# Kernel tuning notes

Measured on AMD Instinct MI355X. Metric: run time of the kernel, lower is better.

## Reference

```python
import jax, jax.numpy as jnp
import numpy as np

N = 3072        # seeds = 3 * batch (src, dst, neg)
K = 64          # num_tokens (sampled neighbors per seed)
C = 128         # edge_dim (mixer channels)
T = 100         # time_dim
ND = 128        # node_dim
ED = 128        # embed_dim
NUM_NODES = 100000
TG = 98304      # total flattened time-gap neighbor indices
L = 2           # num mixer layers
TH = int(K * 0.5)   # token hidden = 32
CH = int(C * 4.0)   # channel hidden = 512
PAD = 0         # PADDED_NODE_ID


def setup_inputs() -> dict:
    key = jax.random.key(0)
    ks = jax.random.split(key, 32)
    inp = {}
    inp['edge_feat'] = jax.random.normal(ks[0], (N, K, C), jnp.float32)
    inp['seed_times'] = jax.random.uniform(ks[1], (N,), jnp.float32) * 1000.0
    inp['nbr_time'] = jax.random.uniform(ks[2], (N, K), jnp.float32) * 1000.0
    inp['node_feat'] = jax.random.normal(ks[3], (NUM_NODES, ND), jnp.float32)
    # Time2Vec frozen frequencies (GraphMixer style)
    inp['time_w'] = jnp.asarray(1.0 / np.power(10.0, np.linspace(0.0, 9.0, T)), jnp.float32)
    s = 0.02
    inp['proj_W'] = jax.random.normal(ks[4], (C + T, C), jnp.float32) * s
    inp['proj_b'] = jnp.zeros((C,), jnp.float32)
    inp['ln1_g'] = jnp.ones((L, C), jnp.float32)
    inp['ln1_b'] = jnp.zeros((L, C), jnp.float32)
    inp['tW1'] = jax.random.normal(ks[5], (L, K, TH), jnp.float32) * s
    inp['tb1'] = jnp.zeros((L, TH), jnp.float32)
    inp['tW2'] = jax.random.normal(ks[6], (L, TH, K), jnp.float32) * s
    inp['tb2'] = jnp.zeros((L, K), jnp.float32)
    inp['ln2_g'] = jnp.ones((L, C), jnp.float32)
    inp['ln2_b'] = jnp.zeros((L, C), jnp.float32)
    inp['cW1'] = jax.random.normal(ks[7], (L, C, CH), jnp.float32) * s
    inp['cb1'] = jnp.zeros((L, CH), jnp.float32)
    inp['cW2'] = jax.random.normal(ks[8], (L, CH, C), jnp.float32) * s
    inp['cb2'] = jnp.zeros((L, C), jnp.float32)
    inp['out_W'] = jax.random.normal(ks[9], (C + ND, ED), jnp.float32) * s
    inp['out_b'] = jnp.zeros((ED,), jnp.float32)
    inp['nbr_nids'] = jax.random.randint(ks[10], (N, K), 0, NUM_NODES, jnp.int32)
    inp['tg_idx'] = jax.random.randint(ks[11], (TG,), 0, NUM_NODES, jnp.int32)
    inp['tg_seg'] = jnp.sort(jax.random.randint(ks[12], (TG,), 0, N, jnp.int32))
    inp['seed_ids'] = jax.random.randint(ks[13], (N,), 0, NUM_NODES, jnp.int32)
    return inp


def _ln(x, g, b):
    m = jnp.mean(x, axis=-1, keepdims=True)
    v = jnp.var(x, axis=-1, keepdims=True)
    return (x - m) * jax.lax.rsqrt(v + 1e-5) * g + b


def reference(edge_feat, seed_times, nbr_time, node_feat, time_w, proj_W, proj_b,
              ln1_g, ln1_b, tW1, tb1, tW2, tb2, ln2_g, ln2_b, cW1, cb1, cW2, cb2,
              out_W, out_b, nbr_nids, tg_idx, tg_seg, seed_ids):
    # Time2Vec on time deltas: [N, K, T]
    dt = seed_times[:, None] - nbr_time
    tfeat = jnp.cos(dt[..., None] * time_w)
    # projection: [N, K, C]
    z = jnp.concatenate([edge_feat, tfeat], axis=-1) @ proj_W + proj_b
    # MLP-Mixer layers (token mixing over K, channel mixing over C)
    for l in range(L):
        h = _ln(z, ln1_g[l], ln1_b[l])
        h = jnp.einsum('nkc,kh->nhc', h, tW1[l]) + tb1[l][None, :, None]
        h = jax.nn.gelu(h)
        h = jnp.einsum('nhc,hk->nkc', h, tW2[l]) + tb2[l][None, :, None]
        z = z + h
        h = _ln(z, ln2_g[l], ln2_b[l])
        h = jax.nn.gelu(h @ cW1[l] + cb1[l]) @ cW2[l] + cb2[l]
        z = z + h
    # masked mean over valid neighbors -> [N, C]
    mask = (nbr_nids != PAD).astype(z.dtype)
    z = jnp.sum(z * mask[..., None], axis=1) / jnp.clip(jnp.sum(mask, axis=1, keepdims=True), 1.0)
    # ragged segment-mean over time-gap neighbors (replaces Python loop)
    counts = jax.ops.segment_sum(jnp.ones((TG,), z.dtype), tg_seg, num_segments=N)
    tg_feat = jax.ops.segment_sum(node_feat[tg_idx], tg_seg, num_segments=N) / jnp.clip(counts, 1.0)[:, None]
    z_node = tg_feat + node_feat[seed_ids]
    return jnp.concatenate([z, z_node], axis=1) @ out_W + out_b
```

## Files before the change

### kernel.cpp

```cpp
#include <hip/hip_runtime.h>
#include <math.h>

#define NS   3072
#define KT   64
#define CC   128
#define TDIM 100
#define TGN  98304
#define TH   32
#define CH   512
#define PS   136
#define PSA  136
#define PSK  72
#define PSH  40

typedef __attribute__((ext_vector_type(8))) short bf16x8;
typedef __attribute__((ext_vector_type(4))) float f32x4;

__device__ __forceinline__ unsigned short f2bf(float f) {
    unsigned int u = __float_as_uint(f);
    return (unsigned short)((u + 0x7FFFu + ((u >> 16) & 1u)) >> 16);
}
__device__ __forceinline__ float fast_exp2(float x) {
    float r; asm("v_exp_f32 %0, %1" : "=v"(r) : "v"(x)); return r;
}
__device__ __forceinline__ float fast_rcp(float x) {
    float r; asm("v_rcp_f32 %0, %1" : "=v"(r) : "v"(x)); return r;
}
__device__ __forceinline__ float fast_cos2pi(float rev) {
    float f = rev - floorf(rev);
    float r; asm("v_cos_f32 %0, %1" : "=v"(r) : "v"(f)); return r;
}
__device__ __forceinline__ unsigned int pk_bf16(float lo, float hi) {
    unsigned int r; asm("v_cvt_pk_bf16_f32 %0, %1, %2" : "=v"(r) : "v"(lo), "v"(hi)); return r;
}
__device__ __forceinline__ float gelu_f(float x) {
    float p = x * x;
    float e = fast_exp2(-x * fmaf(p, 0.1029436f, 2.3022082f));
    return x * fast_rcp(1.0f + e);
}

__global__ __launch_bounds__(256)
void gm_trans(const float* __restrict__ cW1, const float* __restrict__ cW2,
              const float* __restrict__ proj_W,
              unsigned short* __restrict__ cW1Tb, unsigned short* __restrict__ cW2Tb,
              unsigned short* __restrict__ projWTb)
{
    __shared__ float tile[32][33];
    const int bid = blockIdx.x;
    const float* src; unsigned short* dst;
    int R, Cs, oC, tr, tc;
    if (bid < 128) {
        int l = bid >> 6, q = bid & 63; tr = q >> 4; tc = q & 15;
        src = cW1 + l * CC * CH; dst = cW1Tb + l * CH * CC; R = CC; Cs = CH; oC = CC;
    } else if (bid < 256) {
        int b = bid - 128, l = b >> 6, q = b & 63; tr = q & 15; tc = q >> 4;
        src = cW2 + l * CH * CC; dst = cW2Tb + l * CC * CH; R = CH; Cs = CC; oC = CH;
    } else {
        int b = bid - 256; tr = b >> 2; tc = b & 3;
        src = proj_W; dst = projWTb; R = 228; Cs = CC; oC = 256;
    }
    const int tx = threadIdx.x & 31, ty0 = threadIdx.x >> 5;
    #pragma unroll
    for (int i = 0; i < 4; ++i) {
        int ty = ty0 + i * 8;
        int rr = tr * 32 + ty, cc = tc * 32 + tx;
        tile[ty][tx] = (rr < R) ? src[rr * Cs + cc] : 0.0f;
    }
    __syncthreads();
    #pragma unroll
    for (int i = 0; i < 4; ++i) {
        int ty = ty0 + i * 8;
        int orow = tc * 32 + ty, ocol = tr * 32 + tx;
        dst[orow * oC + ocol] = f2bf(tile[tx][ty]);
    }
}

__global__ __launch_bounds__(256)
void gm_prep_small(const float* __restrict__ tW1, const float* __restrict__ tW2,
                   unsigned short* __restrict__ tW1Tb, unsigned short* __restrict__ tW2Tb)
{
    int e = blockIdx.x * 256 + threadIdx.x;
    if (e < 4096) {
        int l = e >> 11, rem = e & 2047, h = rem >> 6, k = rem & 63;
        tW1Tb[e] = f2bf(tW1[(l * KT + k) * TH + h]);
    } else {
        int e2 = e - 4096, l = e2 >> 11, rem = e2 & 2047, k = rem >> 5, h = rem & 31;
        tW2Tb[e2] = f2bf(tW2[(l * TH + h) * KT + k]);
    }
}

__global__ __launch_bounds__(256, 3)
void gm_mixer(const float* __restrict__ edge_feat,
              const float* __restrict__ seed_times,
              const float* __restrict__ nbr_time,
              const float* __restrict__ time_w,
              const float* __restrict__ proj_b,
              const float* __restrict__ ln1_g, const float* __restrict__ ln1_b,
              const float* __restrict__ tb1,   const float* __restrict__ tb2,
              const float* __restrict__ ln2_g, const float* __restrict__ ln2_b,
              const float* __restrict__ cb1,   const float* __restrict__ cb2,
              const int*   __restrict__ nbr_nids,
              const unsigned short* __restrict__ projWTb,
              const unsigned short* __restrict__ tW1Tb,
              const unsigned short* __restrict__ tW2Tb,
              const unsigned short* __restrict__ cW1Tb,
              const unsigned short* __restrict__ cW2Tb,
              float* __restrict__ zmean)
{
    __shared__ short ubuf[17408];
    __shared__ float lnS[256], lnS2[256];
    __shared__ float mArr[KT], rArr[KT], maskArr[KT], dtArr[KT];

    const int n  = blockIdx.x;
    const int t  = threadIdx.x;
    const int w  = t >> 6;
    const int l  = t & 63;
    const int lr = l & 15;
    const int kg = l >> 4;
    const int c0 = w * 32 + lr;
    const int c1 = c0 + 16;

    short* Ab    = ubuf;
    short* LNz1T = ubuf;
    short* G2T   = ubuf + 128 * PSK;
    short* LNzb  = ubuf;
    short* Gb    = ubuf + 64 * PS;

    const f32x4 zero4 = {0.f, 0.f, 0.f, 0.f};
    f32x4 zr[4][2];

    if (t < KT) {
        dtArr[t]   = seed_times[n] - nbr_time[n * KT + t];
        maskArr[t] = (nbr_nids[n * KT + t] != 0) ? 1.0f : 0.0f;
    }
    {
        const float4* ef4 = (const float4*)(edge_feat + (size_t)n * KT * CC);
        #pragma unroll
        for (int it = 0; it < 8; ++it) {
            int i4 = it * 256 + t;
            int k = i4 >> 5, c = (i4 & 31) << 2;
            float4 v = ef4[i4];
            uint2 pk; pk.x = pk_bf16(v.x, v.y); pk.y = pk_bf16(v.z, v.w);
            *(uint2*)&Ab[k * PSA + c] = pk;
        }
    }
    __syncthreads();

    {
        f32x4 acc[4][2];
        #pragma unroll
        for (int mt = 0; mt < 4; ++mt) { acc[mt][0] = zero4; acc[mt][1] = zero4; }
        #pragma unroll
        for (int p = 0; p < 2; ++p) {
            #pragma unroll
            for (int ks = 0; ks < 4; ++ks) {
                const unsigned short* bp = projWTb + (w * 32 + lr) * 256 + p * 128 + ks * 32 + kg * 8;
                bf16x8 b0 = *(const bf16x8*)bp;
                bf16x8 b1 = *(const bf16x8*)(bp + 16 * 256);
                #pragma unroll
                for (int mt = 0; mt < 4; ++mt) {
                    bf16x8 a = *(const bf16x8*)&Ab[(mt * 16 + lr) * PSA + ks * 32 + kg * 8];
                    acc[mt][0] = __builtin_amdgcn_mfma_f32_16x16x32_bf16(a, b0, acc[mt][0], 0, 0, 0);
                    acc[mt][1] = __builtin_amdgcn_mfma_f32_16x16x32_bf16(a, b1, acc[mt][1], 0, 0, 0);
                }
            }
            if (p == 0) {
                __syncthreads();
                #pragma unroll
                for (int it = 0; it < 16; ++it) {
                    int idx = it * 256 + t;
                    int k = idx >> 6, j2 = (idx & 63) << 1;
                    unsigned pk = 0;
                    if (j2 < TDIM) {
                        float dt = dtArr[k];
                        float2 twv = *(const float2*)&time_w[j2];
                        pk = pk_bf16(fast_cos2pi(dt * twv.x * 0.15915494309f),
                                     fast_cos2pi(dt * twv.y * 0.15915494309f));
                    }
                    *(unsigned*)&Ab[k * PSA + j2] = pk;
                }
                __syncthreads();
            }
        }
        #pragma unroll
        for (int mt = 0; mt < 4; ++mt)
            #pragma unroll
            for (int nt = 0; nt < 2; ++nt) {
                float pb = proj_b[nt ? c1 : c0];
                #pragma unroll
                for (int r = 0; r < 4; ++r) zr[mt][nt][r] = acc[mt][nt][r] + pb;
            }
    }

    for (int lay = 0; lay < 2; ++lay) {
        #pragma unroll
        for (int mt = 0; mt < 4; ++mt) {
            f32x4 sv, qv;
            #pragma unroll
            for (int r = 0; r < 4; ++r) {
                float z0 = zr[mt][0][r], z1 = zr[mt][1][r];
                sv[r] = z0 + z1;
                qv[r] = z0 * z0 + z1 * z1;
            }
            #pragma unroll
            for (int d = 1; d < 16; d <<= 1)
                #pragma unroll
                for (int r = 0; r < 4; ++r) {
                    sv[r] += __shfl_xor(sv[r], d);
                    qv[r] += __shfl_xor(qv[r], d);
                }
            if (lr == 0) {
                *(f32x4*)&lnS [w * 64 + mt * 16 + kg * 4] = sv;
                *(f32x4*)&lnS2[w * 64 + mt * 16 + kg * 4] = qv;
            }
        }
        __syncthreads();
        if (t < KT) {
            float s  = lnS [t] + lnS [64 + t] + lnS [128 + t] + lnS [192 + t];
            float s2 = lnS2[t] + lnS2[64 + t] + lnS2[128 + t] + lnS2[192 + t];
            float m = s * (1.0f / CC);
            float var = s2 * (1.0f / CC) - m * m;
            mArr[t] = m; rArr[t] = rsqrtf(var + 1e-5f);
        }
        __syncthreads();

        {
            const float* g1 = ln1_g + lay * CC;
            const float* b1 = ln1_b + lay * CC;
            float gc0 = g1[c0], bc0 = b1[c0], gc1 = g1[c1], bc1 = b1[c1];
            #pragma unroll
            for (int mt = 0; mt < 4; ++mt) {
                f32x4 mv = *(const f32x4*)&mArr[mt * 16 + kg * 4];
                f32x4 rv = *(const f32x4*)&rArr[mt * 16 + kg * 4];
                #pragma unroll
                for (int nt = 0; nt < 2; ++nt) {
                    float gg = nt ? gc1 : gc0, bb = nt ? bc1 : bc0;
                    int c = nt ? c1 : c0;
                    float v0 = (zr[mt][nt][0] - mv[0]) * rv[0] * gg + bb;
                    float v1 = (zr[mt][nt][1] - mv[1]) * rv[1] * gg + bb;
                    float v2 = (zr[mt][nt][2] - mv[2]) * rv[2] * gg + bb;
                    float v3 = (zr[mt][nt][3] - mv[3]) * rv[3] * gg + bb;
                    uint2 pk; pk.x = pk_bf16(v0, v1); pk.y = pk_bf16(v2, v3);
                    *(uint2*)&LNz1T[c * PSK + mt * 16 + kg * 4] = pk;
                }
            }
        }

        {
            f32x4 acc1[2][2];
            #pragma unroll
            for (int mt = 0; mt < 2; ++mt) { acc1[mt][0] = zero4; acc1[mt][1] = zero4; }
            #pragma unroll
            for (int ks = 0; ks < 2; ++ks) {
                bf16x8 bb0 = *(const bf16x8*)&LNz1T[c0 * PSK + ks * 32 + kg * 8];
                bf16x8 bb1 = *(const bf16x8*)&LNz1T[c1 * PSK + ks * 32 + kg * 8];
                #pragma unroll
                for (int mt = 0; mt < 2; ++mt) {
                    bf16x8 a = *(const bf16x8*)&tW1Tb[lay * 2048 + (mt * 16 + lr) * 64 + ks * 32 + kg * 8];
                    acc1[mt][0] = __builtin_amdgcn_mfma_f32_16x16x32_bf16(a, bb0, acc1[mt][0], 0, 0, 0);
                    acc1[mt][1] = __builtin_amdgcn_mfma_f32_16x16x32_bf16(a, bb1, acc1[mt][1], 0, 0, 0);
                }
            }
            #pragma unroll
            for (int mt = 0; mt < 2; ++mt) {
                float4 tbv = *(const float4*)&tb1[lay * TH + mt * 16 + kg * 4];
                #pragma unroll
                for (int nt = 0; nt < 2; ++nt) {
                    int c = nt ? c1 : c0;
                    float g0 = gelu_f(acc1[mt][nt][0] + tbv.x);
                    float g1v = gelu_f(acc1[mt][nt][1] + tbv.y);
                    float g2 = gelu_f(acc1[mt][nt][2] + tbv.z);
                    float g3 = gelu_f(acc1[mt][nt][3] + tbv.w);
                    uint2 pk; pk.x = pk_bf16(g0, g1v); pk.y = pk_bf16(g2, g3);
                    *(uint2*)&G2T[c * PSH + mt * 16 + kg * 4] = pk;
                }
            }
        }
        {
            bf16x8 bb0 = *(const bf16x8*)&G2T[c0 * PSH + kg * 8];
            bf16x8 bb1 = *(const bf16x8*)&G2T[c1 * PSH + kg * 8];
            #pragma unroll
            for (int mt = 0; mt < 4; ++mt) {
                f32x4 a2v0 = zero4, a2v1 = zero4;
                bf16x8 a = *(const bf16x8*)&tW2Tb[lay * 2048 + (mt * 16 + lr) * 32 + kg * 8];
                a2v0 = __builtin_amdgcn_mfma_f32_16x16x32_bf16(a, bb0, a2v0, 0, 0, 0);
                a2v1 = __builtin_amdgcn_mfma_f32_16x16x32_bf16(a, bb1, a2v1, 0, 0, 0);
                float4 t2v = *(const float4*)&tb2[lay * KT + mt * 16 + kg * 4];
                #pragma unroll
                for (int r = 0; r < 4; ++r) {
                    float tb = (r == 0) ? t2v.x : (r == 1) ? t2v.y : (r == 2) ? t2v.z : t2v.w;
                    zr[mt][0][r] += a2v0[r] + tb;
                    zr[mt][1][r] += a2v1[r] + tb;
                }
            }
        }

        #pragma unroll
        for (int mt = 0; mt < 4; ++mt) {
            f32x4 sv, qv;
            #pragma unroll
            for (int r = 0; r < 4; ++r) {
                float z0 = zr[mt][0][r], z1 = zr[mt][1][r];
                sv[r] = z0 + z1;
                qv[r] = z0 * z0 + z1 * z1;
            }
            #pragma unroll
            for (int d = 1; d < 16; d <<= 1)
                #pragma unroll
                for (int r = 0; r < 4; ++r) {
                    sv[r] += __shfl_xor(sv[r], d);
                    qv[r] += __shfl_xor(qv[r], d);
                }
            if (lr == 0) {
                *(f32x4*)&lnS [w * 64 + mt * 16 + kg * 4] = sv;
                *(f32x4*)&lnS2[w * 64 + mt * 16 + kg * 4] = qv;
            }
        }
        __syncthreads();
        if (t < KT) {
            float s  = lnS [t] + lnS [64 + t] + lnS [128 + t] + lnS [192 + t];
            float s2 = lnS2[t] + lnS2[64 + t] + lnS2[128 + t] + lnS2[192 + t];
            float m = s * (1.0f / CC);
            float var = s2 * (1.0f / CC) - m * m;
            mArr[t] = m; rArr[t] = rsqrtf(var + 1e-5f);
        }
        __syncthreads();

        {
            const float* g2 = ln2_g + lay * CC;
            const float* b2 = ln2_b + lay * CC;
            float gc0 = g2[c0], bc0 = b2[c0], gc1 = g2[c1], bc1 = b2[c1];
            const bool odd = lr & 1;
            const int cb = odd ? (c1 - 1) : c0;
            #pragma unroll
            for (int mt = 0; mt < 4; ++mt) {
                f32x4 mv = *(const f32x4*)&mArr[mt * 16 + kg * 4];
                f32x4 rv = *(const f32x4*)&rArr[mt * 16 + kg * 4];
                #pragma unroll
                for (int r = 0; r < 4; ++r) {
                    float v0 = (zr[mt][0][r] - mv[r]) * rv[r] * gc0 + bc0;
                    float v1 = (zr[mt][1][r] - mv[r]) * rv[r] * gc1 + bc1;
                    float s0 = __shfl_xor(v0, 1);
                    float s1 = __shfl_xor(v1, 1);
                    unsigned pka = pk_bf16(v0, s0);
                    unsigned pkb = pk_bf16(s1, v1);
                    unsigned pkv = odd ? pkb : pka;
                    *(unsigned*)&LNzb[(mt * 16 + kg * 4 + r) * PS + cb] = pkv;
                }
            }
        }
        __syncthreads();

        {
            f32x4 accB[4][2];
            #pragma unroll
            for (int mt = 0; mt < 4; ++mt) { accB[mt][0] = zero4; accB[mt][1] = zero4; }

            for (int jc = 0; jc < 4; ++jc) {
                f32x4 accA[4][2];
                #pragma unroll
                for (int mt = 0; mt < 4; ++mt) { accA[mt][0] = zero4; accA[mt][1] = zero4; }
                #pragma unroll
                for (int ks = 0; ks < 4; ++ks) {
                    const unsigned short* w1p = cW1Tb + lay * CH * CC
                                              + (jc * 128 + w * 32 + lr) * CC + ks * 32 + kg * 8;
                    bf16x8 a0 = *(const bf16x8*)w1p;
                    bf16x8 a1 = *(const bf16x8*)(w1p + 16 * CC);
                    #pragma unroll
                    for (int mt = 0; mt < 4; ++mt) {
                        bf16x8 b = *(const bf16x8*)&LNzb[(mt * 16 + lr) * PS + ks * 32 + kg * 8];
                        accA[mt][0] = __builtin_amdgcn_mfma_f32_16x16x32_bf16(a0, b, accA[mt][0], 0, 0, 0);
                        accA[mt][1] = __builtin_amdgcn_mfma_f32_16x16x32_bf16(a1, b, accA[mt][1], 0, 0, 0);
                    }
                }
                #pragma unroll
                for (int nt = 0; nt < 2; ++nt) {
                    int j0 = w * 32 + nt * 16 + kg * 4;
                    float4 cbv = *(const float4*)&cb1[lay * CH + jc * 128 + j0];
                    #pragma unroll
                    for (int mt = 0; mt < 4; ++mt) {
                        float g0 = gelu_f(accA[mt][nt][0] + cbv.x);
                        float g1v = gelu_f(accA[mt][nt][1] + cbv.y);
                        float g2 = gelu_f(accA[mt][nt][2] + cbv.z);
                        float g3 = gelu_f(accA[mt][nt][3] + cbv.w);
                        uint2 pk; pk.x = pk_bf16(g0, g1v); pk.y = pk_bf16(g2, g3);
                        *(uint2*)&Gb[(mt * 16 + lr) * PS + j0] = pk;
                    }
                }
                __syncthreads();
                #pragma unroll
                for (int ks = 0; ks < 4; ++ks) {
                    const unsigned short* w2p = cW2Tb + lay * CC * CH
                                              + (w * 32 + lr) * CH + jc * 128 + ks * 32 + kg * 8;
                    bf16x8 b0 = *(const bf16x8*)w2p;
                    bf16x8 b1 = *(const bf16x8*)(w2p + 16 * CH);
                    #pragma unroll
                    for (int mt = 0; mt < 4; ++mt) {
                        bf16x8 a = *(const bf16x8*)&Gb[(mt * 16 + lr) * PS + ks * 32 + kg * 8];
                        accB[mt][0] = __builtin_amdgcn_mfma_f32_16x16x32_bf16(a, b0, accB[mt][0], 0, 0, 0);
                        accB[mt][1] = __builtin_amdgcn_mfma_f32_16x16x32_bf16(a, b1, accB[mt][1], 0, 0, 0);
                    }
                }
                __syncthreads();
            }
            #pragma unroll
            for (int mt = 0; mt < 4; ++mt)
                #pragma unroll
                for (int nt = 0; nt < 2; ++nt) {
                    float cb = cb2[lay * CC + (nt ? c1 : c0)];
                    #pragma unroll
                    for (int r = 0; r < 4; ++r) zr[mt][nt][r] += accB[mt][nt][r] + cb;
                }
        }
    }

    {
        float msum = 0.f, a0v = 0.f, a1v = 0.f;
        #pragma unroll
        for (int mt = 0; mt < 4; ++mt) {
            f32x4 mk4 = *(const f32x4*)&maskArr[mt * 16 + kg * 4];
            #pragma unroll
            for (int r = 0; r < 4; ++r) {
                msum += mk4[r];
                a0v  += zr[mt][0][r] * mk4[r];
                a1v  += zr[mt][1][r] * mk4[r];
            }
        }
        a0v  += __shfl_xor(a0v, 16);  a0v  += __shfl_xor(a0v, 32);
        a1v  += __shfl_xor(a1v, 16);  a1v  += __shfl_xor(a1v, 32);
        msum += __shfl_xor(msum, 16); msum += __shfl_xor(msum, 32);
        if (kg == 0) {
            float inv = fast_rcp(fmaxf(msum, 1.0f));
            zmean[n * CC + c0] = a0v * inv;
            zmean[n * CC + c1] = a1v * inv;
        }
    }
}

__global__ __launch_bounds__(256)
void gm_out(const float* __restrict__ zmean,
            const float* __restrict__ node_feat,
            const float* __restrict__ out_W,
            const float* __restrict__ out_b,
            const int*   __restrict__ tg_idx,
            const int*   __restrict__ tg_seg,
            const int*   __restrict__ seed_ids,
            float* __restrict__ outp)
{
    __shared__ float redf[8 * 132];
    __shared__ float zmL[CC], znL[CC], oL[2 * CC];
    const int n = blockIdx.x;
    const int t = threadIdx.x;
    const int q = t & 31, g = t >> 5;

    int a = 0, b = TGN;
    while (a < b) { int mm = (a + b) >> 1; if (tg_seg[mm] < n) a = mm + 1; else b = mm; }
    const int lo = a;
    int a2 = lo, b2 = TGN;
    while (a2 < b2) { int mm = (a2 + b2) >> 1; if (tg_seg[mm] < n + 1) a2 = mm + 1; else b2 = mm; }
    const int hi = a2;

    float4 acc = {0.f, 0.f, 0.f, 0.f};
    for (int i = lo + g; i < hi; i += 8) {
        int nid = tg_idx[i];
        const float4* nf = (const float4*)(node_feat + (size_t)nid * CC);
        float4 v = nf[q];
        acc.x += v.x; acc.y += v.y; acc.z += v.z; acc.w += v.w;
    }
    *(float4*)&redf[g * 132 + q * 4] = acc;
    __syncthreads();
    if (t < CC) {
        float s = 0.f;
        #pragma unroll
        for (int gg = 0; gg < 8; ++gg) s += redf[gg * 132 + t];
        float cnt = (float)(hi - lo);
        znL[t] = s / fmaxf(cnt, 1.0f) + node_feat[(size_t)seed_ids[n] * CC + t];
        zmL[t] = zmean[n * CC + t];
    }
    __syncthreads();
    {
        const int c = t & 127, h = t >> 7;
        const float* src = h ? znL : zmL;
        const float* Wp  = out_W + (size_t)h * CC * 128;
        float o = 0.f;
        for (int j = 0; j < CC; ++j) o += src[j] * Wp[j * 128 + c];
        oL[h * 128 + c] = o;
    }
    __syncthreads();
    if (t < CC) outp[n * 128 + t] = oL[t] + oL[CC + t] + out_b[t];
}

extern "C" void kernel_launch(void* const* d_in, const int* in_sizes, int n_in,
                              void* d_out, int out_size, void* d_ws, size_t ws_size,
                              hipStream_t stream)
{
    const float* edge_feat  = (const float*)d_in[0];
    const float* seed_times = (const float*)d_in[1];
    const float* nbr_time   = (const float*)d_in[2];
    const float* node_feat  = (const float*)d_in[3];
    const float* time_w     = (const float*)d_in[4];
    const float* proj_W     = (const float*)d_in[5];
    const float* proj_b     = (const float*)d_in[6];
    const float* ln1_g      = (const float*)d_in[7];
    const float* ln1_b      = (const float*)d_in[8];
    const float* tW1        = (const float*)d_in[9];
    const float* tb1        = (const float*)d_in[10];
    const float* tW2        = (const float*)d_in[11];
    const float* tb2        = (const float*)d_in[12];
    const float* ln2_g      = (const float*)d_in[13];
    const float* ln2_b      = (const float*)d_in[14];
    const float* cW1        = (const float*)d_in[15];
    const float* cb1        = (const float*)d_in[16];
    const float* cW2        = (const float*)d_in[17];
    const float* cb2        = (const float*)d_in[18];
    const float* out_W      = (const float*)d_in[19];
    const float* out_b      = (const float*)d_in[20];
    const int*   nbr_nids   = (const int*)d_in[21];
    const int*   tg_idx     = (const int*)d_in[22];
    const int*   tg_seg     = (const int*)d_in[23];
    const int*   seed_ids   = (const int*)d_in[24];

    char* ws = (char*)d_ws;
    float*          zmean   = (float*)ws;
    unsigned short* projWTb = (unsigned short*)(ws + 1572864);
    unsigned short* tW1Tb   = (unsigned short*)(ws + 1638400);
    unsigned short* tW2Tb   = (unsigned short*)(ws + 1646592);
    unsigned short* cW1Tb   = (unsigned short*)(ws + 1654784);
    unsigned short* cW2Tb   = (unsigned short*)(ws + 1916928);

    gm_trans<<<288, 256, 0, stream>>>(cW1, cW2, proj_W, cW1Tb, cW2Tb, projWTb);
    gm_prep_small<<<32, 256, 0, stream>>>(tW1, tW2, tW1Tb, tW2Tb);
    gm_mixer<<<NS, 256, 0, stream>>>(edge_feat, seed_times, nbr_time, time_w,
                                     proj_b, ln1_g, ln1_b, tb1, tb2, ln2_g, ln2_b,
                                     cb1, cb2, nbr_nids,
                                     projWTb, tW1Tb, tW2Tb, cW1Tb, cW2Tb, zmean);
    gm_out<<<NS, 256, 0, stream>>>(zmean, node_feat, out_W, out_b,
                                   tg_idx, tg_seg, seed_ids, (float*)d_out);
}
```

Measured before the change: 524.0 us.

## Fuse output stage into mixer, merge prep kernels, precompute segment offsets

Merges the two weight-prep kernels into one launch that also precomputes per-seed segment start offsets via binary search. The output gather, segment-mean and final projection are folded into the tail of the mixer kernel, which reuses its shared buffer, so the zmean round-trip through global memory and one launch go away. The mixer's occupancy hint is raised from 3 to 4 blocks per SM, and MFMA loops are wrapped in s_setprio to favour matrix issue. The fused tail adds a serial gather/GEMV phase to each mixer block, and the tighter launch bound may cause register spills.

```diff
diff --git a/kernel.cpp b/kernel.cpp
--- a/kernel.cpp
+++ b/kernel.cpp
@@ -40,13 +40,33 @@
 }
 
 __global__ __launch_bounds__(256)
-void gm_trans(const float* __restrict__ cW1, const float* __restrict__ cW2,
-              const float* __restrict__ proj_W,
-              unsigned short* __restrict__ cW1Tb, unsigned short* __restrict__ cW2Tb,
-              unsigned short* __restrict__ projWTb)
+void gm_prep(const float* __restrict__ cW1, const float* __restrict__ cW2,
+             const float* __restrict__ proj_W,
+             const float* __restrict__ tW1, const float* __restrict__ tW2,
+             const int*   __restrict__ tg_seg,
+             unsigned short* __restrict__ cW1Tb, unsigned short* __restrict__ cW2Tb,
+             unsigned short* __restrict__ projWTb,
+             unsigned short* __restrict__ tW1Tb, unsigned short* __restrict__ tW2Tb,
+             int* __restrict__ seg_lo)
 {
     __shared__ float tile[32][33];
     const int bid = blockIdx.x;
+    if (bid >= 288) {
+        int e = (bid - 288) * 256 + threadIdx.x;
+        if (e < 4096) {
+            int l = e >> 11, rem = e & 2047, h = rem >> 6, k = rem & 63;
+            tW1Tb[e] = f2bf(tW1[(l * KT + k) * TH + h]);
+        } else if (e < 8192) {
+            int e2 = e - 4096, l = e2 >> 11, rem = e2 & 2047, k = rem >> 5, h = rem & 31;
+            tW2Tb[e2] = f2bf(tW2[(l * TH + h) * KT + k]);
+        } else if (e < 8192 + 3073) {
+            int nn = e - 8192;
+            int a = 0, b = TGN;
+            while (a < b) { int mm = (a + b) >> 1; if (tg_seg[mm] < nn) a = mm + 1; else b = mm; }
+            seg_lo[nn] = a;
+        }
+        return;
+    }
     const float* src; unsigned short* dst;
     int R, Cs, oC, tr, tc;
     if (bid < 128) {
@@ -75,21 +95,7 @@
     }
 }
 
-__global__ __launch_bounds__(256)
-void gm_prep_small(const float* __restrict__ tW1, const float* __restrict__ tW2,
-                   unsigned short* __restrict__ tW1Tb, unsigned short* __restrict__ tW2Tb)
-{
-    int e = blockIdx.x * 256 + threadIdx.x;
-    if (e < 4096) {
-        int l = e >> 11, rem = e & 2047, h = rem >> 6, k = rem & 63;
-        tW1Tb[e] = f2bf(tW1[(l * KT + k) * TH + h]);
-    } else {
-        int e2 = e - 4096, l = e2 >> 11, rem = e2 & 2047, k = rem >> 5, h = rem & 31;
-        tW2Tb[e2] = f2bf(tW2[(l * TH + h) * KT + k]);
-    }
-}
-
-__global__ __launch_bounds__(256, 3)
+__global__ __launch_bounds__(256, 4)
 void gm_mixer(const float* __restrict__ edge_feat,
               const float* __restrict__ seed_times,
               const float* __restrict__ nbr_time,
@@ -105,7 +111,13 @@
               const unsigned short* __restrict__ tW2Tb,
               const unsigned short* __restrict__ cW1Tb,
               const unsigned short* __restrict__ cW2Tb,
-              float* __restrict__ zmean)
+              const float* __restrict__ node_feat,
+              const float* __restrict__ out_W,
+              const float* __restrict__ out_b,
+              const int*   __restrict__ tg_idx,
+              const int*   __restrict__ seed_ids,
+              const int*   __restrict__ seg_lo,
+              float* __restrict__ outp)
 {
     __shared__ short ubuf[17408];
     __shared__ float lnS[256], lnS2[256];
@@ -360,6 +372,7 @@
                 f32x4 accA[4][2];
                 #pragma unroll
                 for (int mt = 0; mt < 4; ++mt) { accA[mt][0] = zero4; accA[mt][1] = zero4; }
+                __builtin_amdgcn_s_setprio(1);
                 #pragma unroll
                 for (int ks = 0; ks < 4; ++ks) {
                     const unsigned short* w1p = cW1Tb + lay * CH * CC
@@ -373,6 +386,7 @@
                         accA[mt][1] = __builtin_amdgcn_mfma_f32_16x16x32_bf16(a1, b, accA[mt][1], 0, 0, 0);
                     }
                 }
+                __builtin_amdgcn_s_setprio(0);
                 #pragma unroll
                 for (int nt = 0; nt < 2; ++nt) {
                     int j0 = w * 32 + nt * 16 + kg * 4;
@@ -388,6 +402,7 @@
                     }
                 }
                 __syncthreads();
+                __builtin_amdgcn_s_setprio(1);
                 #pragma unroll
                 for (int ks = 0; ks < 4; ++ks) {
                     const unsigned short* w2p = cW2Tb + lay * CC * CH
@@ -401,6 +416,7 @@
                         accB[mt][1] = __builtin_amdgcn_mfma_f32_16x16x32_bf16(a, b1, accB[mt][1], 0, 0, 0);
                     }
                 }
+                __builtin_amdgcn_s_setprio(0);
                 __syncthreads();
             }
             #pragma unroll
@@ -413,6 +429,11 @@
                 }
         }
     }
+
+    float* redf = (float*)ubuf;
+    float* zmL  = redf + 8 * 132;
+    float* znL  = zmL + 128;
+    float* oL   = znL + 128;
 
     {
         float msum = 0.f, a0v = 0.f, a1v = 0.f;
@@ -431,43 +452,22 @@
         msum += __shfl_xor(msum, 16); msum += __shfl_xor(msum, 32);
         if (kg == 0) {
             float inv = fast_rcp(fmaxf(msum, 1.0f));
-            zmean[n * CC + c0] = a0v * inv;
-            zmean[n * CC + c1] = a1v * inv;
-        }
-    }
-}
-
-__global__ __launch_bounds__(256)
-void gm_out(const float* __restrict__ zmean,
-            const float* __restrict__ node_feat,
-            const float* __restrict__ out_W,
-            const float* __restrict__ out_b,
-            const int*   __restrict__ tg_idx,
-            const int*   __restrict__ tg_seg,
-            const int*   __restrict__ seed_ids,
-            float* __restrict__ outp)
-{
-    __shared__ float redf[8 * 132];
-    __shared__ float zmL[CC], znL[CC], oL[2 * CC];
-    const int n = blockIdx.x;
-    const int t = threadIdx.x;
-    const int q = t & 31, g = t >> 5;
-
-    int a = 0, b = TGN;
-    while (a < b) { int mm = (a + b) >> 1; if (tg_seg[mm] < n) a = mm + 1; else b = mm; }
-    const int lo = a;
-    int a2 = lo, b2 = TGN;
-    while (a2 < b2) { int mm = (a2 + b2) >> 1; if (tg_seg[mm] < n + 1) a2 = mm + 1; else b2 = mm; }
-    const int hi = a2;
-
-    float4 acc = {0.f, 0.f, 0.f, 0.f};
-    for (int i = lo + g; i < hi; i += 8) {
-        int nid = tg_idx[i];
-        const float4* nf = (const float4*)(node_feat + (size_t)nid * CC);
-        float4 v = nf[q];
-        acc.x += v.x; acc.y += v.y; acc.z += v.z; acc.w += v.w;
-    }
-    *(float4*)&redf[g * 132 + q * 4] = acc;
+            zmL[c0] = a0v * inv;
+            zmL[c1] = a1v * inv;
+        }
+    }
+
+    const int lo = seg_lo[n], hi = seg_lo[n + 1];
+    {
+        const int q = t & 31, g = t >> 5;
+        float4 acc = {0.f, 0.f, 0.f, 0.f};
+        for (int i = lo + g; i < hi; i += 8) {
+            const float4* nf = (const float4*)(node_feat + (size_t)tg_idx[i] * CC);
+            float4 v = nf[q];
+            acc.x += v.x; acc.y += v.y; acc.z += v.z; acc.w += v.w;
+        }
+        *(float4*)&redf[g * 132 + q * 4] = acc;
+    }
     __syncthreads();
     if (t < CC) {
         float s = 0.f;
@@ -475,7 +475,6 @@
         for (int gg = 0; gg < 8; ++gg) s += redf[gg * 132 + t];
         float cnt = (float)(hi - lo);
         znL[t] = s / fmaxf(cnt, 1.0f) + node_feat[(size_t)seed_ids[n] * CC + t];
-        zmL[t] = zmean[n * CC + t];
     }
     __syncthreads();
     {
@@ -521,19 +520,19 @@
     const int*   seed_ids   = (const int*)d_in[24];
 
     char* ws = (char*)d_ws;
-    float*          zmean   = (float*)ws;
-    unsigned short* projWTb = (unsigned short*)(ws + 1572864);
-    unsigned short* tW1Tb   = (unsigned short*)(ws + 1638400);
-    unsigned short* tW2Tb   = (unsigned short*)(ws + 1646592);
-    unsigned short* cW1Tb   = (unsigned short*)(ws + 1654784);
-    unsigned short* cW2Tb   = (unsigned short*)(ws + 1916928);
-
-    gm_trans<<<288, 256, 0, stream>>>(cW1, cW2, proj_W, cW1Tb, cW2Tb, projWTb);
-    gm_prep_small<<<32, 256, 0, stream>>>(tW1, tW2, tW1Tb, tW2Tb);
+    int*            seg_lo  = (int*)ws;
+    unsigned short* projWTb = (unsigned short*)(ws + 16384);
+    unsigned short* tW1Tb   = (unsigned short*)(ws + 81920);
+    unsigned short* tW2Tb   = (unsigned short*)(ws + 90112);
+    unsigned short* cW1Tb   = (unsigned short*)(ws + 98304);
+    unsigned short* cW2Tb   = (unsigned short*)(ws + 360448);
+
+    gm_prep<<<333, 256, 0, stream>>>(cW1, cW2, proj_W, tW1, tW2, tg_seg,
+                                     cW1Tb, cW2Tb, projWTb, tW1Tb, tW2Tb, seg_lo);
     gm_mixer<<<NS, 256, 0, stream>>>(edge_feat, seed_times, nbr_time, time_w,
                                      proj_b, ln1_g, ln1_b, tb1, tb2, ln2_g, ln2_b,
                                      cb1, cb2, nbr_nids,
-                                     projWTb, tW1Tb, tW2Tb, cW1Tb, cW2Tb, zmean);
-    gm_out<<<NS, 256, 0, stream>>>(zmean, node_feat, out_W, out_b,
-                                   tg_idx, tg_seg, seed_ids, (float*)d_out);
-}
+                                     projWTb, tW1Tb, tW2Tb, cW1Tb, cW2Tb,
+                                     node_feat, out_W, out_b, tg_idx, seed_ids, seg_lo,
+                                     (float*)d_out);
+}
```

New measurement: 569.4 us. 8.7% more time.
